# Optimization experiments

Measured on AMD Instinct MI355X. Metric: run time of the kernel, lower is better.

Reference implementation:

```python
import jax, jax.numpy as jnp
import numpy as np

B, C, W, H, D = 2, 256, 32, 32, 32
CH = C // 2  # 128
LN_EPS = 1e-5


def _spatial_pool(x, wm, bm):
    # x: [B,C,W,H,D]; wm: [C]; bm: scalar. 1x1x1 conv C->1 == channel dot.
    b, c = x.shape[0], x.shape[1]
    xf = x.reshape(b, c, -1)                       # [B,C,N]
    mask = jnp.einsum('bcn,c->bn', xf, wm) + bm    # [B,N]
    attn = jax.nn.softmax(mask, axis=1)            # softmax over spatial N
    return jnp.einsum('bcn,bn->bc', xf, attn)      # [B,C] weighted-sum pool


def _channel_add(ctx, w1, b1, g, be, w2, b2):
    # 1x1 conv C->C/2, LayerNorm over C/2, ReLU, 1x1 conv C/2->C
    h = ctx @ w1.T + b1                            # [B,CH]
    mu = jnp.mean(h, axis=-1, keepdims=True)
    var = jnp.mean((h - mu) ** 2, axis=-1, keepdims=True)
    h = (h - mu) * jax.lax.rsqrt(var + LN_EPS) * g + be
    h = jax.nn.relu(h)
    return h @ w2.T + b2                           # [B,C]


def setup_inputs() -> dict:
    key = jax.random.key(0)
    ks = jax.random.split(key, 20)
    s = 0.02
    d = {
        'preds_S': jax.random.normal(ks[0], (B, C, W, H, D), jnp.float32),
        'preds_T': jax.random.normal(ks[1], (B, C, W, H, D), jnp.float32),
        'wm_s': jax.random.normal(ks[2], (C,), jnp.float32) * s,
        'bm_s': jnp.zeros((), jnp.float32),
        'wm_t': jax.random.normal(ks[3], (C,), jnp.float32) * s,
        'bm_t': jnp.zeros((), jnp.float32),
        'w1_s': jax.random.normal(ks[4], (CH, C), jnp.float32) * s,
        'b1_s': jnp.zeros((CH,), jnp.float32),
        'g_s': jnp.ones((CH,), jnp.float32),
        'be_s': jnp.zeros((CH,), jnp.float32),
        'w2_s': jax.random.normal(ks[5], (C, CH), jnp.float32) * s,
        'b2_s': jnp.zeros((C,), jnp.float32),
        'w1_t': jax.random.normal(ks[6], (CH, C), jnp.float32) * s,
        'b1_t': jnp.zeros((CH,), jnp.float32),
        'g_t': jnp.ones((CH,), jnp.float32),
        'be_t': jnp.zeros((CH,), jnp.float32),
        'w2_t': jax.random.normal(ks[7], (C, CH), jnp.float32) * s,
        'b2_t': jnp.zeros((C,), jnp.float32),
    }
    return d


def reference(preds_S, preds_T, wm_s, bm_s, wm_t, bm_t,
              w1_s, b1_s, g_s, be_s, w2_s, b2_s,
              w1_t, b1_t, g_t, be_t, w2_t, b2_t):
    ctx_s = _spatial_pool(preds_S, wm_s, bm_s)     # [B,C]
    ctx_t = _spatial_pool(preds_T, wm_t, bm_t)
    add_s = _channel_add(ctx_s, w1_s, b1_s, g_s, be_s, w2_s, b2_s)  # [B,C]
    add_t = _channel_add(ctx_t, w1_t, b1_t, g_t, be_t, w2_t, b2_t)
    out_s = preds_S + add_s[:, :, None, None, None]
    out_t = preds_T + add_t[:, :, None, None, None]
    diff = out_s - out_t
    return jnp.sum(diff * diff) / preds_S.shape[0]
```

## Files before the change

kernel.cpp:

```cpp
#include <hip/hip_runtime.h>
#include <math.h>

#define Bc   2
#define Cc   256
#define Nn   32768
#define CHc  128
#define LN_EPS 1e-5f

#define TN    64
#define TPB   512
#define NQ    16
#define CG    32
#define CPG   8
#define GRIDX (Nn / TN)
#define NSLOT 32

__global__ __launch_bounds__(TPB, 2) void gc_fused(
    const float* __restrict__ S, const float* __restrict__ T,
    const float* __restrict__ wms, const float* __restrict__ bms,
    const float* __restrict__ wmt, const float* __restrict__ bmt,
    float* __restrict__ ctxnum,
    float* __restrict__ rowsum,
    float* __restrict__ den,
    float* __restrict__ sumsq) {
  const int b    = blockIdx.y;
  const int tid  = threadIdx.x;
  const int nq   = tid & (NQ - 1);
  const int cg   = tid >> 4;
  const int wv   = tid >> 6;
  const int lane = tid & 63;
  const int sub  = lane & 15;
  const int c0   = cg * CPG;
  const int n0   = blockIdx.x * TN + nq * 4;
  const int slot = blockIdx.x & (NSLOT - 1);

  __shared__ float4 mredw[2][8][NQ];
  __shared__ float  sqred[8];

  const float bS = bms[0];
  const float bT = bmt[0];

  const float* Sp = S + ((size_t)b * Cc + c0) * Nn + n0;
  const float* Tp = T + ((size_t)b * Cc + c0) * Nn + n0;

  float4 s4[CPG], t4[CPG];
#pragma unroll
  for (int i = 0; i < CPG; ++i) s4[i] = *(const float4*)(Sp + (size_t)i * Nn);
#pragma unroll
  for (int i = 0; i < CPG; ++i) t4[i] = *(const float4*)(Tp + (size_t)i * Nn);

  float wS[CPG], wT[CPG];
#pragma unroll
  for (int i = 0; i < CPG; ++i) { wS[i] = wms[c0 + i]; wT[i] = wmt[c0 + i]; }

  float4 ms = make_float4(0.f, 0.f, 0.f, 0.f);
  float4 mt = make_float4(0.f, 0.f, 0.f, 0.f);
#pragma unroll
  for (int i = 0; i < CPG; ++i) {
    ms.x += wS[i] * s4[i].x; ms.y += wS[i] * s4[i].y;
    ms.z += wS[i] * s4[i].z; ms.w += wS[i] * s4[i].w;
    mt.x += wT[i] * t4[i].x; mt.y += wT[i] * t4[i].y;
    mt.z += wT[i] * t4[i].z; mt.w += wT[i] * t4[i].w;
  }

#pragma unroll
  for (int m = 16; m <= 32; m <<= 1) {
    ms.x += __shfl_xor(ms.x, m); ms.y += __shfl_xor(ms.y, m);
    ms.z += __shfl_xor(ms.z, m); ms.w += __shfl_xor(ms.w, m);
    mt.x += __shfl_xor(mt.x, m); mt.y += __shfl_xor(mt.y, m);
    mt.z += __shfl_xor(mt.z, m); mt.w += __shfl_xor(mt.w, m);
  }
  if (lane < NQ) { mredw[0][wv][nq] = ms; mredw[1][wv][nq] = mt; }

  float pd[CPG];
  float sq = 0.f;
#pragma unroll
  for (int i = 0; i < CPG; ++i) {
    const float dx = s4[i].x - t4[i].x, dy = s4[i].y - t4[i].y;
    const float dz = s4[i].z - t4[i].z, dw = s4[i].w - t4[i].w;
    pd[i] = dx + dy + dz + dw;
    sq += dx * dx + dy * dy + dz * dz + dw * dw;
  }
#pragma unroll
  for (int m = 1; m <= 8; m <<= 1) {
#pragma unroll
    for (int i = 0; i < CPG; ++i) pd[i] += __shfl_xor(pd[i], m);
  }
#pragma unroll
  for (int m = 1; m < 64; m <<= 1) sq += __shfl_xor(sq, m);
  if (lane == 0) sqred[wv] = sq;

  __syncthreads();

  float4 Ms = make_float4(0.f, 0.f, 0.f, 0.f);
  float4 Mt = make_float4(0.f, 0.f, 0.f, 0.f);
#pragma unroll
  for (int w = 0; w < 8; ++w) {
    const float4 a = mredw[0][w][nq];
    Ms.x += a.x; Ms.y += a.y; Ms.z += a.z; Ms.w += a.w;
    const float4 c = mredw[1][w][nq];
    Mt.x += c.x; Mt.y += c.y; Mt.z += c.z; Mt.w += c.w;
  }
  float4 es, et;
  es.x = __expf(Ms.x + bS); es.y = __expf(Ms.y + bS);
  es.z = __expf(Ms.z + bS); es.w = __expf(Ms.w + bS);
  et.x = __expf(Mt.x + bT); et.y = __expf(Mt.y + bT);
  et.z = __expf(Mt.z + bT); et.w = __expf(Mt.w + bT);

  float dens = es.x + es.y + es.z + es.w;
  float dent = et.x + et.y + et.z + et.w;
  float ps[CPG], pt[CPG];
#pragma unroll
  for (int i = 0; i < CPG; ++i) {
    ps[i] = s4[i].x * es.x + s4[i].y * es.y + s4[i].z * es.z + s4[i].w * es.w;
    pt[i] = t4[i].x * et.x + t4[i].y * et.y + t4[i].z * et.z + t4[i].w * et.w;
  }
#pragma unroll
  for (int m = 1; m <= 8; m <<= 1) {
#pragma unroll
    for (int i = 0; i < CPG; ++i) {
      ps[i] += __shfl_xor(ps[i], m);
      pt[i] += __shfl_xor(pt[i], m);
    }
    dens += __shfl_xor(dens, m);
    dent += __shfl_xor(dent, m);
  }

  const int k = sub & 7;
  float vs = ps[0], vt = pt[0], vd = pd[0];
#pragma unroll
  for (int i = 1; i < CPG; ++i) {
    const bool m = (k == i);
    vs = m ? ps[i] : vs;
    vt = m ? pt[i] : vt;
    vd = m ? pd[i] : vd;
  }

  if (sub < 8) {
    atomicAdd(&ctxnum[(((size_t)slot * 2 + 0) * Bc + b) * Cc + c0 + k], vs);
    atomicAdd(&rowsum[((size_t)slot * Bc + b) * Cc + c0 + k], vd);
  } else {
    atomicAdd(&ctxnum[(((size_t)slot * 2 + 1) * Bc + b) * Cc + c0 + k], vt);
  }
  if (tid == 0) {
    atomicAdd(&den[slot * 4 + 0 * Bc + b], dens);
    atomicAdd(&den[slot * 4 + 1 * Bc + b], dent);
  }
  if (tid == 64) {
    float v = 0.f;
#pragma unroll
    for (int w = 0; w < 8; ++w) v += sqred[w];
    atomicAdd(&sumsq[slot], v);
  }
}

__global__ __launch_bounds__(1024) void gc_k4a_mlp(
    const float* __restrict__ ctxr, const float* __restrict__ den,
    const float* __restrict__ w1s, const float* __restrict__ b1s,
    const float* __restrict__ gs,  const float* __restrict__ bes,
    const float* __restrict__ w2s, const float* __restrict__ b2s,
    const float* __restrict__ w1t, const float* __restrict__ b1t,
    const float* __restrict__ gt,  const float* __restrict__ bet,
    const float* __restrict__ w2t, const float* __restrict__ b2t,
    float* __restrict__ addv) {
  const int tt  = blockIdx.x >> 1;
  const int b   = blockIdx.x & 1;
  const int tid = threadIdx.x;

  const float* w1 = tt ? w1t : w1s;
  const float* b1 = tt ? b1t : b1s;
  const float* g  = tt ? gt  : gs;
  const float* be = tt ? bet : bes;
  const float* w2 = tt ? w2t : w2s;
  const float* b2 = tt ? b2t : b2s;

  __shared__ float cxs[Cc];
  __shared__ float part[1024];
  __shared__ float hbuf[CHc];
  __shared__ float hr[CHc];
  __shared__ float2 red2[128];
  __shared__ float mu_s, rstd_s;

  if (tid < Cc) {
    float num = 0.f, dn = 0.f;
#pragma unroll
    for (int kk = 0; kk < NSLOT; ++kk) {
      num += ctxr[(((size_t)kk * 2 + tt) * Bc + b) * Cc + tid];
      dn  += den[kk * 4 + tt * Bc + b];
    }
    cxs[tid] = num / dn;
  }
  __syncthreads();

  {
    const int j = tid >> 3, s = tid & 7;
    const float* wr = w1 + j * Cc + s * 32;
    const float4* cx4 = (const float4*)(cxs + s * 32);
    float acc = 0.f;
#pragma unroll
    for (int kk = 0; kk < 8; ++kk) {
      const float4 w = *(const float4*)(wr + kk * 4);
      const float4 x = cx4[kk];
      acc += w.x * x.x + w.y * x.y + w.z * x.z + w.w * x.w;
    }
    part[tid] = acc;
  }
  __syncthreads();
  if (tid < CHc) {
    float h = b1[tid];
#pragma unroll
    for (int q = 0; q < 8; ++q) h += part[tid * 8 + q];
    hbuf[tid] = h;
  }
  __syncthreads();

  if (tid < CHc) {
    const float v = hbuf[tid];
    red2[tid] = make_float2(v, v * v);
  }
  __syncthreads();
  for (int s = 64; s > 0; s >>= 1) {
    if (tid < s) {
      red2[tid].x += red2[tid + s].x;
      red2[tid].y += red2[tid + s].y;
    }
    __syncthreads();
  }
  if (tid == 0) {
    const float mu = red2[0].x / (float)CHc;
    const float var = red2[0].y / (float)CHc - mu * mu;
    mu_s = mu;
    rstd_s = rsqrtf(var + LN_EPS);
  }
  __syncthreads();
  if (tid < CHc) {
    const float v = (hbuf[tid] - mu_s) * rstd_s * g[tid] + be[tid];
    hr[tid] = v > 0.f ? v : 0.f;
  }
  __syncthreads();

  {
    const int c = tid >> 2, q = tid & 3;
    const float* wr = w2 + c * CHc + q * 32;
    const float4* h4 = (const float4*)(hr + q * 32);
    float acc = 0.f;
#pragma unroll
    for (int kk = 0; kk < 8; ++kk) {
      const float4 w = *(const float4*)(wr + kk * 4);
      const float4 x = h4[kk];
      acc += w.x * x.x + w.y * x.y + w.z * x.z + w.w * x.w;
    }
    part[tid] = acc;
  }
  __syncthreads();
  if (tid < Cc) {
    float acc = b2[tid];
#pragma unroll
    for (int q = 0; q < 4; ++q) acc += part[tid * 4 + q];
    addv[((size_t)tt * Bc + b) * Cc + tid] = acc;
  }
}

__global__ __launch_bounds__(256) void gc_k4b_final(
    const float* __restrict__ addv, const float* __restrict__ rowsum,
    const float* __restrict__ sumsq, float* __restrict__ out) {
  const int tid = threadIdx.x;
  __shared__ float red[256];
  float part = 0.f;
  for (int job = tid; job < Bc * Cc; job += 256) {
    const int c = job & (Cc - 1);
    const int b = job >> 8;
    const float delta = addv[((size_t)0 * Bc + b) * Cc + c] -
                        addv[((size_t)1 * Bc + b) * Cc + c];
    float rs = 0.f;
#pragma unroll
    for (int k = 0; k < NSLOT; ++k)
      rs += rowsum[((size_t)k * Bc + b) * Cc + c];
    part += 2.f * delta * rs + (float)Nn * delta * delta;
  }
  red[tid] = part;
  __syncthreads();
  for (int s = 128; s > 0; s >>= 1) {
    if (tid < s) red[tid] += red[tid + s];
    __syncthreads();
  }
  if (tid == 0) {
    float sq = 0.f;
#pragma unroll
    for (int k = 0; k < NSLOT; ++k) sq += sumsq[k];
    out[0] = (red[0] + sq) / (float)Bc;
  }
}

extern "C" void kernel_launch(void* const* d_in, const int* in_sizes, int n_in,
                              void* d_out, int out_size, void* d_ws,
                              size_t ws_size, hipStream_t stream) {
  const float* S   = (const float*)d_in[0];
  const float* T   = (const float*)d_in[1];
  const float* wms = (const float*)d_in[2];
  const float* bms = (const float*)d_in[3];
  const float* wmt = (const float*)d_in[4];
  const float* bmt = (const float*)d_in[5];
  const float* w1s = (const float*)d_in[6];
  const float* b1s = (const float*)d_in[7];
  const float* gs  = (const float*)d_in[8];
  const float* bes = (const float*)d_in[9];
  const float* w2s = (const float*)d_in[10];
  const float* b2s = (const float*)d_in[11];
  const float* w1t = (const float*)d_in[12];
  const float* b1t = (const float*)d_in[13];
  const float* gt  = (const float*)d_in[14];
  const float* bet = (const float*)d_in[15];
  const float* w2t = (const float*)d_in[16];
  const float* b2t = (const float*)d_in[17];
  float* out = (float*)d_out;

  float* ws     = (float*)d_ws;
  float* ctxnum = ws;
  float* rowsum = ctxnum + NSLOT * 2 * Bc * Cc;
  float* den    = rowsum + NSLOT * Bc * Cc;
  float* sumsq  = den + NSLOT * 4;
  float* addv   = sumsq + NSLOT;

  hipMemsetAsync(d_ws, 0,
                 (NSLOT * (2 * Bc * Cc + Bc * Cc + 4 + 1)) * sizeof(float),
                 stream);

  gc_fused<<<dim3(GRIDX, Bc), TPB, 0, stream>>>(S, T, wms, bms, wmt, bmt,
                                                ctxnum, rowsum, den, sumsq);
  gc_k4a_mlp<<<4, 1024, 0, stream>>>(ctxnum, den, w1s, b1s, gs, bes, w2s, b2s,
                                     w1t, b1t, gt, bet, w2t, b2t, addv);
  gc_k4b_final<<<1, 256, 0, stream>>>(addv, rowsum, sumsq, out);
}
```

Baseline: 192.6 us.

## Loop each fused block over four spatial tiles with double-buffered loads

The fused pooling kernel now has each block process four 32-wide spatial tiles with 4 channels per thread, prefetching the next tile's S/T registers while computing the current one. Per-channel partial sums go through padded shared-memory tables and are accumulated across iterations, so each block issues one atomic per channel instead of one per tile. This cuts the global atomic count, shrinks the grid by a factor of four and raises the occupancy hint to 4 blocks per CU. In exchange it adds extra __syncthreads per iteration and about 27KB of shared memory per block, which could limit the occupancy actually reached.

```diff
diff --git a/kernel.cpp b/kernel.cpp
--- a/kernel.cpp
+++ b/kernel.cpp
@@ -7,15 +7,15 @@
 #define CHc  128
 #define LN_EPS 1e-5f
 
-#define TN    64
+#define TN    32
+#define ITERS 4
 #define TPB   512
-#define NQ    16
-#define CG    32
-#define CPG   8
-#define GRIDX (Nn / TN)
+#define NQ    8
+#define CPG   4
+#define GRIDX (Nn / (TN * ITERS))
 #define NSLOT 32
 
-__global__ __launch_bounds__(TPB, 2) void gc_fused(
+__global__ __launch_bounds__(TPB, 4) void gc_fused(
     const float* __restrict__ S, const float* __restrict__ T,
     const float* __restrict__ wms, const float* __restrict__ bms,
     const float* __restrict__ wmt, const float* __restrict__ bmt,
@@ -26,127 +26,131 @@
   const int b    = blockIdx.y;
   const int tid  = threadIdx.x;
   const int nq   = tid & (NQ - 1);
-  const int cg   = tid >> 4;
+  const int cg   = tid >> 3;
   const int wv   = tid >> 6;
   const int lane = tid & 63;
-  const int sub  = lane & 15;
   const int c0   = cg * CPG;
-  const int n0   = blockIdx.x * TN + nq * 4;
   const int slot = blockIdx.x & (NSLOT - 1);
+  const int nbase = blockIdx.x * (ITERS * TN) + nq * 4;
 
   __shared__ float4 mredw[2][8][NQ];
+  __shared__ float  creds[Cc * 9];
+  __shared__ float  credt[Cc * 9];
+  __shared__ float  credd[Cc * 9];
   __shared__ float  sqred[8];
 
   const float bS = bms[0];
   const float bT = bmt[0];
 
-  const float* Sp = S + ((size_t)b * Cc + c0) * Nn + n0;
-  const float* Tp = T + ((size_t)b * Cc + c0) * Nn + n0;
-
-  float4 s4[CPG], t4[CPG];
-#pragma unroll
-  for (int i = 0; i < CPG; ++i) s4[i] = *(const float4*)(Sp + (size_t)i * Nn);
-#pragma unroll
-  for (int i = 0; i < CPG; ++i) t4[i] = *(const float4*)(Tp + (size_t)i * Nn);
+  const float* Sp = S + ((size_t)b * Cc + c0) * Nn + nbase;
+  const float* Tp = T + ((size_t)b * Cc + c0) * Nn + nbase;
 
   float wS[CPG], wT[CPG];
 #pragma unroll
   for (int i = 0; i < CPG; ++i) { wS[i] = wms[c0 + i]; wT[i] = wmt[c0 + i]; }
 
-  float4 ms = make_float4(0.f, 0.f, 0.f, 0.f);
-  float4 mt = make_float4(0.f, 0.f, 0.f, 0.f);
-#pragma unroll
-  for (int i = 0; i < CPG; ++i) {
-    ms.x += wS[i] * s4[i].x; ms.y += wS[i] * s4[i].y;
-    ms.z += wS[i] * s4[i].z; ms.w += wS[i] * s4[i].w;
-    mt.x += wT[i] * t4[i].x; mt.y += wT[i] * t4[i].y;
-    mt.z += wT[i] * t4[i].z; mt.w += wT[i] * t4[i].w;
-  }
-
-#pragma unroll
-  for (int m = 16; m <= 32; m <<= 1) {
-    ms.x += __shfl_xor(ms.x, m); ms.y += __shfl_xor(ms.y, m);
-    ms.z += __shfl_xor(ms.z, m); ms.w += __shfl_xor(ms.w, m);
-    mt.x += __shfl_xor(mt.x, m); mt.y += __shfl_xor(mt.y, m);
-    mt.z += __shfl_xor(mt.z, m); mt.w += __shfl_xor(mt.w, m);
-  }
-  if (lane < NQ) { mredw[0][wv][nq] = ms; mredw[1][wv][nq] = mt; }
-
-  float pd[CPG];
-  float sq = 0.f;
-#pragma unroll
-  for (int i = 0; i < CPG; ++i) {
-    const float dx = s4[i].x - t4[i].x, dy = s4[i].y - t4[i].y;
-    const float dz = s4[i].z - t4[i].z, dw = s4[i].w - t4[i].w;
-    pd[i] = dx + dy + dz + dw;
-    sq += dx * dx + dy * dy + dz * dz + dw * dw;
-  }
-#pragma unroll
-  for (int m = 1; m <= 8; m <<= 1) {
-#pragma unroll
-    for (int i = 0; i < CPG; ++i) pd[i] += __shfl_xor(pd[i], m);
-  }
+  float accS = 0.f, accT = 0.f, accR = 0.f;
+  float dens = 0.f, dent = 0.f, sq = 0.f;
+
+  float4 sA[CPG], tA[CPG], sB[CPG], tB[CPG];
+
+#pragma unroll
+  for (int i = 0; i < CPG; ++i) sA[i] = *(const float4*)(Sp + (size_t)i * Nn);
+#pragma unroll
+  for (int i = 0; i < CPG; ++i) tA[i] = *(const float4*)(Tp + (size_t)i * Nn);
+
+#define GC_BODY(CS, CT, NS, NT, IT, HASNEXT)                                  \
+  do {                                                                        \
+    if (HASNEXT) {                                                            \
+      _Pragma("unroll") for (int i = 0; i < CPG; ++i)                         \
+          NS[i] = *(const float4*)(Sp + (size_t)i * Nn + ((IT) + 1) * TN);    \
+      _Pragma("unroll") for (int i = 0; i < CPG; ++i)                         \
+          NT[i] = *(const float4*)(Tp + (size_t)i * Nn + ((IT) + 1) * TN);    \
+    }                                                                         \
+    float4 ms = make_float4(0.f, 0.f, 0.f, 0.f);                              \
+    float4 mt = make_float4(0.f, 0.f, 0.f, 0.f);                              \
+    _Pragma("unroll") for (int i = 0; i < CPG; ++i) {                         \
+      ms.x += wS[i] * CS[i].x; ms.y += wS[i] * CS[i].y;                       \
+      ms.z += wS[i] * CS[i].z; ms.w += wS[i] * CS[i].w;                       \
+      mt.x += wT[i] * CT[i].x; mt.y += wT[i] * CT[i].y;                       \
+      mt.z += wT[i] * CT[i].z; mt.w += wT[i] * CT[i].w;                       \
+    }                                                                         \
+                         \
+    _Pragma("unroll") for (int m = 8; m <= 32; m <<= 1) {                     \
+      ms.x += __shfl_xor(ms.x, m); ms.y += __shfl_xor(ms.y, m);               \
+      ms.z += __shfl_xor(ms.z, m); ms.w += __shfl_xor(ms.w, m);               \
+      mt.x += __shfl_xor(mt.x, m); mt.y += __shfl_xor(mt.y, m);               \
+      mt.z += __shfl_xor(mt.z, m); mt.w += __shfl_xor(mt.w, m);               \
+    }                                                                         \
+    if (lane < NQ) { mredw[0][wv][lane] = ms; mredw[1][wv][lane] = mt; }      \
+    __syncthreads();                           \
+    float4 Ms = make_float4(0.f, 0.f, 0.f, 0.f);                              \
+    float4 Mt = make_float4(0.f, 0.f, 0.f, 0.f);                              \
+    _Pragma("unroll") for (int w = 0; w < 8; ++w) {                           \
+      const float4 a = mredw[0][w][nq];                                       \
+      Ms.x += a.x; Ms.y += a.y; Ms.z += a.z; Ms.w += a.w;                     \
+      const float4 c = mredw[1][w][nq];                                       \
+      Mt.x += c.x; Mt.y += c.y; Mt.z += c.z; Mt.w += c.w;                     \
+    }                                                                         \
+    float4 es, et;                                                            \
+    es.x = __expf(Ms.x + bS); es.y = __expf(Ms.y + bS);                       \
+    es.z = __expf(Ms.z + bS); es.w = __expf(Ms.w + bS);                       \
+    et.x = __expf(Mt.x + bT); et.y = __expf(Mt.y + bT);                       \
+    et.z = __expf(Mt.z + bT); et.w = __expf(Mt.w + bT);                       \
+    dens += es.x + es.y + es.z + es.w;                                        \
+    dent += et.x + et.y + et.z + et.w;                                        \
+    _Pragma("unroll") for (int i = 0; i < CPG; ++i) {                         \
+      creds[(c0 + i) * 9 + nq] = CS[i].x * es.x + CS[i].y * es.y +            \
+                                 CS[i].z * es.z + CS[i].w * es.w;             \
+      credt[(c0 + i) * 9 + nq] = CT[i].x * et.x + CT[i].y * et.y +            \
+                                 CT[i].z * et.z + CT[i].w * et.w;             \
+      const float dx = CS[i].x - CT[i].x, dy = CS[i].y - CT[i].y;             \
+      const float dz = CS[i].z - CT[i].z, dw = CS[i].w - CT[i].w;             \
+      credd[(c0 + i) * 9 + nq] = dx + dy + dz + dw;                           \
+      sq += dx * dx + dy * dy + dz * dz + dw * dw;                            \
+    }                                                                         \
+    __syncthreads();                        \
+    if (tid < Cc) {                                                           \
+      float a = 0.f, r = 0.f;                                                 \
+      _Pragma("unroll") for (int k = 0; k < NQ; ++k) {                        \
+        a += creds[tid * 9 + k];                                              \
+        r += credd[tid * 9 + k];                                              \
+      }                                                                       \
+      accS += a; accR += r;                                                   \
+    } else {                                                                  \
+      float t = 0.f;                                                          \
+      _Pragma("unroll") for (int k = 0; k < NQ; ++k)                          \
+          t += credt[(tid - Cc) * 9 + k];                                     \
+      accT += t;                                                              \
+    }                                                                         \
+  } while (0)
+
+  GC_BODY(sA, tA, sB, tB, 0, 1);
+  GC_BODY(sB, tB, sA, tA, 1, 1);
+  GC_BODY(sA, tA, sB, tB, 2, 1);
+  GC_BODY(sB, tB, sA, tA, 3, 0);
+#undef GC_BODY
+
 #pragma unroll
   for (int m = 1; m < 64; m <<= 1) sq += __shfl_xor(sq, m);
   if (lane == 0) sqred[wv] = sq;
-
-  __syncthreads();
-
-  float4 Ms = make_float4(0.f, 0.f, 0.f, 0.f);
-  float4 Mt = make_float4(0.f, 0.f, 0.f, 0.f);
-#pragma unroll
-  for (int w = 0; w < 8; ++w) {
-    const float4 a = mredw[0][w][nq];
-    Ms.x += a.x; Ms.y += a.y; Ms.z += a.z; Ms.w += a.w;
-    const float4 c = mredw[1][w][nq];
-    Mt.x += c.x; Mt.y += c.y; Mt.z += c.z; Mt.w += c.w;
-  }
-  float4 es, et;
-  es.x = __expf(Ms.x + bS); es.y = __expf(Ms.y + bS);
-  es.z = __expf(Ms.z + bS); es.w = __expf(Ms.w + bS);
-  et.x = __expf(Mt.x + bT); et.y = __expf(Mt.y + bT);
-  et.z = __expf(Mt.z + bT); et.w = __expf(Mt.w + bT);
-
-  float dens = es.x + es.y + es.z + es.w;
-  float dent = et.x + et.y + et.z + et.w;
-  float ps[CPG], pt[CPG];
-#pragma unroll
-  for (int i = 0; i < CPG; ++i) {
-    ps[i] = s4[i].x * es.x + s4[i].y * es.y + s4[i].z * es.z + s4[i].w * es.w;
-    pt[i] = t4[i].x * et.x + t4[i].y * et.y + t4[i].z * et.z + t4[i].w * et.w;
-  }
-#pragma unroll
-  for (int m = 1; m <= 8; m <<= 1) {
-#pragma unroll
-    for (int i = 0; i < CPG; ++i) {
-      ps[i] += __shfl_xor(ps[i], m);
-      pt[i] += __shfl_xor(pt[i], m);
-    }
+#pragma unroll
+  for (int m = 1; m <= 4; m <<= 1) {
     dens += __shfl_xor(dens, m);
     dent += __shfl_xor(dent, m);
   }
-
-  const int k = sub & 7;
-  float vs = ps[0], vt = pt[0], vd = pd[0];
-#pragma unroll
-  for (int i = 1; i < CPG; ++i) {
-    const bool m = (k == i);
-    vs = m ? ps[i] : vs;
-    vt = m ? pt[i] : vt;
-    vd = m ? pd[i] : vd;
-  }
-
-  if (sub < 8) {
-    atomicAdd(&ctxnum[(((size_t)slot * 2 + 0) * Bc + b) * Cc + c0 + k], vs);
-    atomicAdd(&rowsum[((size_t)slot * Bc + b) * Cc + c0 + k], vd);
+  __syncthreads();
+
+  if (tid < Cc) {
+    atomicAdd(&ctxnum[(((size_t)slot * 2 + 0) * Bc + b) * Cc + tid], accS);
+    atomicAdd(&rowsum[((size_t)slot * Bc + b) * Cc + tid], accR);
   } else {
-    atomicAdd(&ctxnum[(((size_t)slot * 2 + 1) * Bc + b) * Cc + c0 + k], vt);
+    atomicAdd(&ctxnum[(((size_t)slot * 2 + 1) * Bc + b) * Cc + (tid - Cc)],
+              accT);
   }
   if (tid == 0) {
     atomicAdd(&den[slot * 4 + 0 * Bc + b], dens);
     atomicAdd(&den[slot * 4 + 1 * Bc + b], dent);
-  }
-  if (tid == 64) {
     float v = 0.f;
 #pragma unroll
     for (int w = 0; w < 8; ++w) v += sqred[w];
```

New measurement: 219.2 us. 13.8% more time.

## Process two spatial tiles per block with prefetch and LDS cross-thread reduction

Applied to the files above, without the earlier changes.

Each block now handles two 64-wide spatial tiles in a loop, halving the grid and the number of global atomics per element. The next tile's loads are issued while the current tile is being reduced, and the per-channel partial sums move from shuffle reductions plus select chains into padded shared-memory arrays summed by one thread per channel. In exchange the kernel uses about 52KB of extra LDS, adds more barriers per iteration, and keeps more registers live during the prefetch. These costs may reduce occupancy under the two-blocks-per-CU launch bound.

```diff
diff --git a/kernel.cpp b/kernel.cpp
--- a/kernel.cpp
+++ b/kernel.cpp
@@ -8,11 +8,11 @@
 #define LN_EPS 1e-5f
 
 #define TN    64
+#define ITERS 2
 #define TPB   512
 #define NQ    16
-#define CG    32
 #define CPG   8
-#define GRIDX (Nn / TN)
+#define GRIDX (Nn / (TN * ITERS))
 #define NSLOT 32
 
 __global__ __launch_bounds__(TPB, 2) void gc_fused(
@@ -29,19 +29,28 @@
   const int cg   = tid >> 4;
   const int wv   = tid >> 6;
   const int lane = tid & 63;
-  const int sub  = lane & 15;
   const int c0   = cg * CPG;
-  const int n0   = blockIdx.x * TN + nq * 4;
   const int slot = blockIdx.x & (NSLOT - 1);
+  const int nbase = blockIdx.x * (ITERS * TN) + nq * 4;
 
   __shared__ float4 mredw[2][8][NQ];
+  __shared__ float  creds[Cc * 17];
+  __shared__ float  credt[Cc * 17];
+  __shared__ float  credd[Cc * 17];
   __shared__ float  sqred[8];
 
   const float bS = bms[0];
   const float bT = bmt[0];
 
-  const float* Sp = S + ((size_t)b * Cc + c0) * Nn + n0;
-  const float* Tp = T + ((size_t)b * Cc + c0) * Nn + n0;
+  const float* Sp = S + ((size_t)b * Cc + c0) * Nn + nbase;
+  const float* Tp = T + ((size_t)b * Cc + c0) * Nn + nbase;
+
+  float wS[CPG], wT[CPG];
+#pragma unroll
+  for (int i = 0; i < CPG; ++i) { wS[i] = wms[c0 + i]; wT[i] = wmt[c0 + i]; }
+
+  float accS = 0.f, accT = 0.f, accR = 0.f;
+  float dens = 0.f, dent = 0.f, sq = 0.f;
 
   float4 s4[CPG], t4[CPG];
 #pragma unroll
@@ -49,104 +58,100 @@
 #pragma unroll
   for (int i = 0; i < CPG; ++i) t4[i] = *(const float4*)(Tp + (size_t)i * Nn);
 
-  float wS[CPG], wT[CPG];
-#pragma unroll
-  for (int i = 0; i < CPG; ++i) { wS[i] = wms[c0 + i]; wT[i] = wmt[c0 + i]; }
-
-  float4 ms = make_float4(0.f, 0.f, 0.f, 0.f);
-  float4 mt = make_float4(0.f, 0.f, 0.f, 0.f);
-#pragma unroll
-  for (int i = 0; i < CPG; ++i) {
-    ms.x += wS[i] * s4[i].x; ms.y += wS[i] * s4[i].y;
-    ms.z += wS[i] * s4[i].z; ms.w += wS[i] * s4[i].w;
-    mt.x += wT[i] * t4[i].x; mt.y += wT[i] * t4[i].y;
-    mt.z += wT[i] * t4[i].z; mt.w += wT[i] * t4[i].w;
-  }
-
-#pragma unroll
-  for (int m = 16; m <= 32; m <<= 1) {
-    ms.x += __shfl_xor(ms.x, m); ms.y += __shfl_xor(ms.y, m);
-    ms.z += __shfl_xor(ms.z, m); ms.w += __shfl_xor(ms.w, m);
-    mt.x += __shfl_xor(mt.x, m); mt.y += __shfl_xor(mt.y, m);
-    mt.z += __shfl_xor(mt.z, m); mt.w += __shfl_xor(mt.w, m);
-  }
-  if (lane < NQ) { mredw[0][wv][nq] = ms; mredw[1][wv][nq] = mt; }
-
-  float pd[CPG];
-  float sq = 0.f;
-#pragma unroll
-  for (int i = 0; i < CPG; ++i) {
-    const float dx = s4[i].x - t4[i].x, dy = s4[i].y - t4[i].y;
-    const float dz = s4[i].z - t4[i].z, dw = s4[i].w - t4[i].w;
-    pd[i] = dx + dy + dz + dw;
-    sq += dx * dx + dy * dy + dz * dz + dw * dw;
-  }
-#pragma unroll
-  for (int m = 1; m <= 8; m <<= 1) {
-#pragma unroll
-    for (int i = 0; i < CPG; ++i) pd[i] += __shfl_xor(pd[i], m);
-  }
+  for (int it = 0; it < ITERS; ++it) {
+    float4 ms = make_float4(0.f, 0.f, 0.f, 0.f);
+    float4 mt = make_float4(0.f, 0.f, 0.f, 0.f);
+#pragma unroll
+    for (int i = 0; i < CPG; ++i) {
+      ms.x += wS[i] * s4[i].x; ms.y += wS[i] * s4[i].y;
+      ms.z += wS[i] * s4[i].z; ms.w += wS[i] * s4[i].w;
+      mt.x += wT[i] * t4[i].x; mt.y += wT[i] * t4[i].y;
+      mt.z += wT[i] * t4[i].z; mt.w += wT[i] * t4[i].w;
+    }
+#pragma unroll
+    for (int m = 16; m <= 32; m <<= 1) {
+      ms.x += __shfl_xor(ms.x, m); ms.y += __shfl_xor(ms.y, m);
+      ms.z += __shfl_xor(ms.z, m); ms.w += __shfl_xor(ms.w, m);
+      mt.x += __shfl_xor(mt.x, m); mt.y += __shfl_xor(mt.y, m);
+      mt.z += __shfl_xor(mt.z, m); mt.w += __shfl_xor(mt.w, m);
+    }
+    if (lane < NQ) { mredw[0][wv][nq] = ms; mredw[1][wv][nq] = mt; }
+
+    __syncthreads();
+
+    float4 Ms = make_float4(0.f, 0.f, 0.f, 0.f);
+    float4 Mt = make_float4(0.f, 0.f, 0.f, 0.f);
+#pragma unroll
+    for (int w = 0; w < 8; ++w) {
+      const float4 a = mredw[0][w][nq];
+      Ms.x += a.x; Ms.y += a.y; Ms.z += a.z; Ms.w += a.w;
+      const float4 c = mredw[1][w][nq];
+      Mt.x += c.x; Mt.y += c.y; Mt.z += c.z; Mt.w += c.w;
+    }
+    float4 es, et;
+    es.x = __expf(Ms.x + bS); es.y = __expf(Ms.y + bS);
+    es.z = __expf(Ms.z + bS); es.w = __expf(Ms.w + bS);
+    et.x = __expf(Mt.x + bT); et.y = __expf(Mt.y + bT);
+    et.z = __expf(Mt.z + bT); et.w = __expf(Mt.w + bT);
+    dens += es.x + es.y + es.z + es.w;
+    dent += et.x + et.y + et.z + et.w;
+
+    const int nextoff = (it + 1) * TN;
+    const bool hasnext = (it + 1 < ITERS);
+#pragma unroll
+    for (int i = 0; i < CPG; ++i) {
+      creds[(c0 + i) * 17 + nq] =
+          s4[i].x * es.x + s4[i].y * es.y + s4[i].z * es.z + s4[i].w * es.w;
+      credt[(c0 + i) * 17 + nq] =
+          t4[i].x * et.x + t4[i].y * et.y + t4[i].z * et.z + t4[i].w * et.w;
+      const float dx = s4[i].x - t4[i].x, dy = s4[i].y - t4[i].y;
+      const float dz = s4[i].z - t4[i].z, dw = s4[i].w - t4[i].w;
+      credd[(c0 + i) * 17 + nq] = dx + dy + dz + dw;
+      sq += dx * dx + dy * dy + dz * dz + dw * dw;
+      if (hasnext) {
+        s4[i] = *(const float4*)(Sp + (size_t)i * Nn + nextoff);
+        t4[i] = *(const float4*)(Tp + (size_t)i * Nn + nextoff);
+      }
+    }
+
+    __syncthreads();
+
+    if (tid < Cc) {
+      float a = 0.f, r = 0.f;
+#pragma unroll
+      for (int k = 0; k < NQ; ++k) {
+        a += creds[tid * 17 + k];
+        r += credd[tid * 17 + k];
+      }
+      accS += a; accR += r;
+    } else {
+      float t = 0.f;
+#pragma unroll
+      for (int k = 0; k < NQ; ++k) t += credt[(tid - Cc) * 17 + k];
+      accT += t;
+    }
+  }
+
 #pragma unroll
   for (int m = 1; m < 64; m <<= 1) sq += __shfl_xor(sq, m);
   if (lane == 0) sqred[wv] = sq;
-
-  __syncthreads();
-
-  float4 Ms = make_float4(0.f, 0.f, 0.f, 0.f);
-  float4 Mt = make_float4(0.f, 0.f, 0.f, 0.f);
-#pragma unroll
-  for (int w = 0; w < 8; ++w) {
-    const float4 a = mredw[0][w][nq];
-    Ms.x += a.x; Ms.y += a.y; Ms.z += a.z; Ms.w += a.w;
-    const float4 c = mredw[1][w][nq];
-    Mt.x += c.x; Mt.y += c.y; Mt.z += c.z; Mt.w += c.w;
-  }
-  float4 es, et;
-  es.x = __expf(Ms.x + bS); es.y = __expf(Ms.y + bS);
-  es.z = __expf(Ms.z + bS); es.w = __expf(Ms.w + bS);
-  et.x = __expf(Mt.x + bT); et.y = __expf(Mt.y + bT);
-  et.z = __expf(Mt.z + bT); et.w = __expf(Mt.w + bT);
-
-  float dens = es.x + es.y + es.z + es.w;
-  float dent = et.x + et.y + et.z + et.w;
-  float ps[CPG], pt[CPG];
-#pragma unroll
-  for (int i = 0; i < CPG; ++i) {
-    ps[i] = s4[i].x * es.x + s4[i].y * es.y + s4[i].z * es.z + s4[i].w * es.w;
-    pt[i] = t4[i].x * et.x + t4[i].y * et.y + t4[i].z * et.z + t4[i].w * et.w;
-  }
 #pragma unroll
   for (int m = 1; m <= 8; m <<= 1) {
-#pragma unroll
-    for (int i = 0; i < CPG; ++i) {
-      ps[i] += __shfl_xor(ps[i], m);
-      pt[i] += __shfl_xor(pt[i], m);
-    }
     dens += __shfl_xor(dens, m);
     dent += __shfl_xor(dent, m);
   }
-
-  const int k = sub & 7;
-  float vs = ps[0], vt = pt[0], vd = pd[0];
-#pragma unroll
-  for (int i = 1; i < CPG; ++i) {
-    const bool m = (k == i);
-    vs = m ? ps[i] : vs;
-    vt = m ? pt[i] : vt;
-    vd = m ? pd[i] : vd;
-  }
-
-  if (sub < 8) {
-    atomicAdd(&ctxnum[(((size_t)slot * 2 + 0) * Bc + b) * Cc + c0 + k], vs);
-    atomicAdd(&rowsum[((size_t)slot * Bc + b) * Cc + c0 + k], vd);
+  __syncthreads();
+
+  if (tid < Cc) {
+    atomicAdd(&ctxnum[(((size_t)slot * 2 + 0) * Bc + b) * Cc + tid], accS);
+    atomicAdd(&rowsum[((size_t)slot * Bc + b) * Cc + tid], accR);
   } else {
-    atomicAdd(&ctxnum[(((size_t)slot * 2 + 1) * Bc + b) * Cc + c0 + k], vt);
+    atomicAdd(&ctxnum[(((size_t)slot * 2 + 1) * Bc + b) * Cc + (tid - Cc)],
+              accT);
   }
   if (tid == 0) {
     atomicAdd(&den[slot * 4 + 0 * Bc + b], dens);
     atomicAdd(&den[slot * 4 + 1 * Bc + b], dent);
-  }
-  if (tid == 64) {
     float v = 0.f;
 #pragma unroll
     for (int w = 0; w < 8; ++w) v += sqred[w];
```

Result: no change. 195.4 us (+1.5%).
